# Performance work log

Measured on AMD Instinct MI355X. Metric: run time of the kernel, lower is better.

## Reference

```python
import jax, jax.numpy as jnp
import numpy as np

D_EMB = 1024
N_HEAD = 16
D_K = D_EMB // N_HEAD


def setup_inputs() -> dict:
    key = jax.random.key(0)
    ks = jax.random.split(key, 11)
    B, S = 2, 2048
    s = 1.0 / np.sqrt(D_EMB)
    inp = {
        'Q': jax.random.normal(ks[0], (B, S, D_EMB), jnp.float32),
        'K': jax.random.normal(ks[1], (B, S, D_EMB), jnp.float32),
        'V': jax.random.normal(ks[2], (B, S, D_EMB), jnp.float32),
        'W_Q': jax.random.normal(ks[3], (D_EMB, D_EMB), jnp.float32) * s,
        'b_Q': jax.random.normal(ks[4], (D_EMB,), jnp.float32) * s,
        'W_K': jax.random.normal(ks[5], (D_EMB, D_EMB), jnp.float32) * s,
        'b_K': jax.random.normal(ks[6], (D_EMB,), jnp.float32) * s,
        'W_V': jax.random.normal(ks[7], (D_EMB, D_EMB), jnp.float32) * s,
        'b_V': jax.random.normal(ks[8], (D_EMB,), jnp.float32) * s,
        'W_O': jax.random.normal(ks[9], (D_EMB, D_EMB), jnp.float32) * s,
        'b_O': jax.random.normal(ks[10], (D_EMB,), jnp.float32) * s,
    }
    return inp


def _heads(x):
    # [B, S, D] -> [B, H, S, d_k]
    B, S, _ = x.shape
    return x.reshape(B, S, N_HEAD, D_K).transpose(0, 2, 1, 3)


def reference(Q, K, V, W_Q, b_Q, W_K, b_K, W_V, b_V, W_O, b_O):
    q = _heads(Q @ W_Q.T + b_Q)
    k = _heads(K @ W_K.T + b_K)
    v = _heads(V @ W_V.T + b_V)
    scale = 1.0 / jnp.sqrt(jnp.asarray(D_K, q.dtype))
    scores = jnp.einsum('bhqd,bhkd->bhqk', q, k) * scale  # [B,H,S,S]
    probs = jax.nn.softmax(scores, axis=-1)
    attn = jnp.einsum('bhqk,bhkd->bhqd', probs, v)
    B, H, S, d = attn.shape
    attn = attn.transpose(0, 2, 1, 3).reshape(B, S, H * d)
    return attn @ W_O.T + b_O
```

## Files before the change

### kernel.cpp

```cpp
#include <hip/hip_runtime.h>
#include <cstdint>
#include <cstddef>

#define S_LEN 2048
#define NH    16
#define DKH   64
#define DEMB  1024
#define MTOT  4096
#define SLAB  (32 * S_LEN * DKH)

typedef float f32x4 __attribute__((ext_vector_type(4)));
typedef __bf16 bf16x8 __attribute__((ext_vector_type(8)));
typedef _Float16 f16;
typedef f16 f16x2 __attribute__((ext_vector_type(2)));
typedef f16 f16x4 __attribute__((ext_vector_type(4)));
typedef f16 f16x8 __attribute__((ext_vector_type(8)));
typedef unsigned short u16;
typedef unsigned int u32;
typedef u16 u16x8 __attribute__((ext_vector_type(8)));
typedef u16 u16x4 __attribute__((ext_vector_type(4)));
typedef u32 u32x4 __attribute__((ext_vector_type(4)));

static __device__ __forceinline__ u16 f2bf(float f) {
  u32 u = __builtin_bit_cast(u32, f);
  u += 0x7fffu + ((u >> 16) & 1u);
  return (u16)(u >> 16);
}
static __device__ __forceinline__ float bf2f(u16 b) {
  return __builtin_bit_cast(float, ((u32)b) << 16);
}
static __device__ __forceinline__ bf16x8 ldfrag(const u16* p) {
  return __builtin_bit_cast(bf16x8, *(const u16x8*)p);
}
static __device__ __forceinline__ f16x8 ldfragh8(const u16* p) {
  return __builtin_bit_cast(f16x8, *(const u16x8*)p);
}
static __device__ __forceinline__ f32x4 mfma16(bf16x8 a, bf16x8 b, f32x4 c) {
  return __builtin_amdgcn_mfma_f32_16x16x32_bf16(a, b, c, 0, 0, 0);
}
static __device__ __forceinline__ f32x4 mfmah32(f16x8 a, f16x8 b, f32x4 c) {
  return __builtin_amdgcn_mfma_f32_16x16x32_f16(a, b, c, 0, 0, 0);
}
static __device__ __forceinline__ void gl2lds16(const void* g, void* l) {
  __builtin_amdgcn_global_load_lds((__attribute__((address_space(1))) void*)g,
                                   (__attribute__((address_space(3))) void*)l,
                                   16, 0, 0);
}
static __device__ __forceinline__ u32 pkh2(float a, float b) {
  return __builtin_bit_cast(u32, __builtin_amdgcn_cvt_pkrtz(a, b));
}
static __device__ __forceinline__ f16x4 pkh4(float a, float b, float c, float d) {
  f16x2 lo = __builtin_bit_cast(f16x2, __builtin_amdgcn_cvt_pkrtz(a, b));
  f16x2 hi = __builtin_bit_cast(f16x2, __builtin_amdgcn_cvt_pkrtz(c, d));
  return __builtin_shufflevector(lo, hi, 0, 1, 2, 3);
}

#define SCL_Q (0.125f * 1.44269504088896340736f)

__global__ __launch_bounds__(256) void cvt_all(
    const float* __restrict__ wq, const float* __restrict__ wk,
    const float* __restrict__ wv, const float* __restrict__ wo,
    const float* __restrict__ q, const float* __restrict__ k,
    const float* __restrict__ v, u16* __restrict__ dW, u16* __restrict__ dA) {
  int b = blockIdx.x;
  const float* s; u16* d;
  if (b < 4096) {
    const int seg = b >> 10;
    s = (seg == 0) ? wq : (seg == 1) ? wk : (seg == 2) ? wv : wo;
    d = dW + (size_t)seg * (DEMB * DEMB);
    b &= 1023;
  } else {
    const int bb = b - 4096;
    const int seg = bb >> 12;
    s = (seg == 0) ? q : (seg == 1) ? k : v;
    d = dA + (size_t)seg * ((size_t)MTOT * DEMB);
    b = bb & 4095;
  }
  const int i = (b * 256 + threadIdx.x) * 4;
  f32x4 f = *(const f32x4*)(s + i);
  u16x4 o;
  o[0] = f2bf(f[0]); o[1] = f2bf(f[1]); o[2] = f2bf(f[2]); o[3] = f2bf(f[3]);
  *(u16x4*)(d + i) = o;
}

__global__ __launch_bounds__(256) void qkv_gemm(
    const u16* __restrict__ qin, const u16* __restrict__ kin,
    const u16* __restrict__ vin, const u16* __restrict__ W,
    const float* __restrict__ bq, const float* __restrict__ bk,
    const float* __restrict__ bv,
    u16* __restrict__ qh, u16* __restrict__ kh, u16* __restrict__ vt) {
  __shared__ __align__(16) u16 sA0[128 * 32], sA1[128 * 32];
  __shared__ __align__(16) u16 sB0[128 * 32], sB1[128 * 32];
  const int t = threadIdx.x;
  const int l = t & 63, w = t >> 6;
  const int ll = l & 15, lg = l >> 4;
  const int orig = blockIdx.x + 24 * blockIdx.y;
  const int xcd = orig & 7, q = orig >> 3;
  const int nb = q >> 2;
  const int mb = xcd * 4 + (q & 3);
  const int which = nb >> 3;
  const u16* A = (which == 0) ? qin : ((which == 1) ? kin : vin);
  const int wr = (w >> 1) * 64, wc = (w & 1) * 64;

  f32x4 acc[4][4] = {};

  auto stg = [&](int kt, u16* dA, u16* dB) {
    const int k0 = kt * 32;
#pragma unroll
    for (int i = 0; i < 2; ++i) {
      const int c = i * 256 + t;
      const int row = c >> 2;
      const int gc = (c & 3) ^ ((row >> 1) & 3);
      gl2lds16(A + (size_t)(mb * 128 + row) * DEMB + k0 + gc * 8, dA + c * 8);
      gl2lds16(W + (size_t)(nb * 128 + row) * DEMB + k0 + gc * 8, dB + c * 8);
    }
  };

  auto comp = [&](const u16* cA, const u16* cB) {
    bf16x8 af[4], bfr[4];
#pragma unroll
    for (int i2 = 0; i2 < 4; ++i2) {
      const int row = wr + i2 * 16 + ll;
      af[i2] = ldfrag(&cA[row * 32 + (lg ^ ((row >> 1) & 3)) * 8]);
    }
#pragma unroll
    for (int j2 = 0; j2 < 4; ++j2) {
      const int row = wc + j2 * 16 + ll;
      bfr[j2] = ldfrag(&cB[row * 32 + (lg ^ ((row >> 1) & 3)) * 8]);
    }
#pragma unroll
    for (int i2 = 0; i2 < 4; ++i2)
#pragma unroll
      for (int j2 = 0; j2 < 4; ++j2)
        acc[i2][j2] = mfma16(af[i2], bfr[j2], acc[i2][j2]);
  };

  stg(0, sA0, sB0);
  __syncthreads();
  for (int kt2 = 0; kt2 < 16; ++kt2) {
    stg(2 * kt2 + 1, sA1, sB1);
    comp(sA0, sB0);
    __syncthreads();
    if (kt2 < 15) stg(2 * kt2 + 2, sA0, sB0);
    comp(sA1, sB1);
    __syncthreads();
  }

  const float* bias = (which == 0) ? bq : ((which == 1) ? bk : bv);
  const int b = (mb * 128) >> 11;

  if (which == 2) {
#pragma unroll
    for (int j2 = 0; j2 < 4; ++j2) {
      const int nl = (nb * 128 + wc + j2 * 16 + ll) & 1023;
      const int h = nl >> 6, dk = nl & 63;
      const float bb = bias[nl];
      u16* base = vt + ((size_t)((b * NH + h) * DKH + dk)) * S_LEN;
#pragma unroll
      for (int i2 = 0; i2 < 4; ++i2) {
        const int s = (mb * 128 + wr + i2 * 16 + lg * 4) & 2047;
        const f16x4 pk = pkh4(acc[i2][j2][0] + bb, acc[i2][j2][1] + bb,
                              acc[i2][j2][2] + bb, acc[i2][j2][3] + bb);
        *(u16x4*)&base[s] = __builtin_bit_cast(u16x4, pk);
      }
    }
  } else {
    u16* outp = (which == 0) ? qh : kh;
    const float scl = (which == 0) ? SCL_Q : 1.0f;
#pragma unroll
    for (int j2 = 0; j2 < 4; ++j2) {
      const int nl = (nb * 128 + wc + j2 * 16 + ll) & 1023;
      const int h = nl >> 6, dk = nl & 63;
      const float bb = bias[nl];
#pragma unroll
      for (int i2 = 0; i2 < 4; ++i2) {
#pragma unroll
        for (int r = 0; r < 4; ++r) {
          const int s = (mb * 128 + wr + i2 * 16 + lg * 4 + r) & 2047;
          const float val = (acc[i2][j2][r] + bb) * scl;
          outp[((size_t)((b * NH + h) * S_LEN + s)) * DKH + dk] = f2bf(val);
        }
      }
    }
  }
}

__global__ __launch_bounds__(512, 4) void attn_kernel(
    const u16* __restrict__ qh, const u16* __restrict__ kh,
    const u16* __restrict__ vt, u16* __restrict__ opart,
    float* __restrict__ lpart) {
  __shared__ __align__(16) u16 sK0[64 * 64], sK1[64 * 64];
  __shared__ __align__(16) u16 sV0[64 * 64], sV1[64 * 64];
  const int t = threadIdx.x;
  const int l = t & 63, w = t >> 6;
  const int ll = l & 15, lg = l >> 4;
  const int qb = blockIdx.x >> 1;
  const int ks = blockIdx.x & 1;
  const int q_blk = qb * 256;
  const int bh = blockIdx.y;

  bf16x8 aq[2][2];
#pragma unroll
  for (int qt = 0; qt < 2; ++qt) {
    const u16* qbase =
        qh + ((size_t)bh * S_LEN + q_blk + w * 32 + qt * 16 + ll) * DKH;
    aq[qt][0] = ldfrag(qbase + lg * 8);
    aq[qt][1] = ldfrag(qbase + 32 + lg * 8);
  }

  f32x4 oT[2][4] = {};
  float l_part[2] = {0.f, 0.f};

  const int strow = t >> 3;
  const int sgc = (t & 7) ^ (strow & 7);
  const u16* kstg =
      kh + ((size_t)bh * S_LEN + ks * 1024 + strow) * DKH + sgc * 8;
  const u16* vstg =
      vt + ((size_t)bh * DKH + strow) * S_LEN + ks * 1024 + sgc * 8;

  auto stg = [&](int kt, u16* dK, u16* dV) {
    gl2lds16(kstg + (size_t)kt * 64 * DKH, dK + t * 8);
    gl2lds16(vstg + kt * 64, dV + t * 8);
  };

  auto compute = [&](const u16* cK, const u16* cV) {
#pragma unroll
    for (int pr = 0; pr < 2; ++pr) {
      u32 pw0[4], pw1[4];
#pragma unroll
      for (int h = 0; h < 2; ++h) {
        const int krow = (pr * 2 + h) * 16 + ll;
        const bf16x8 ak0 = ldfrag(&cK[krow * 64 + (lg ^ (ll & 7)) * 8]);
        const bf16x8 ak1 = ldfrag(&cK[krow * 64 + ((4 + lg) ^ (ll & 7)) * 8]);
        f32x4 s0 = {}, s1 = {};
        s0 = mfma16(ak0, aq[0][0], s0);
        s0 = mfma16(ak1, aq[0][1], s0);
        s1 = mfma16(ak0, aq[1][0], s1);
        s1 = mfma16(ak1, aq[1][1], s1);
        {
          const float p0 = __builtin_amdgcn_exp2f(s0[0]);
          const float p1 = __builtin_amdgcn_exp2f(s0[1]);
          const float p2 = __builtin_amdgcn_exp2f(s0[2]);
          const float p3 = __builtin_amdgcn_exp2f(s0[3]);
          l_part[0] += (p0 + p1) + (p2 + p3);
          if (h == 0) { pw0[0] = pkh2(p0, p1); pw0[1] = pkh2(p2, p3); }
          else        { pw0[2] = pkh2(p0, p1); pw0[3] = pkh2(p2, p3); }
        }
        {
          const float p0 = __builtin_amdgcn_exp2f(s1[0]);
          const float p1 = __builtin_amdgcn_exp2f(s1[1]);
          const float p2 = __builtin_amdgcn_exp2f(s1[2]);
          const float p3 = __builtin_amdgcn_exp2f(s1[3]);
          l_part[1] += (p0 + p1) + (p2 + p3);
          if (h == 0) { pw1[0] = pkh2(p0, p1); pw1[1] = pkh2(p2, p3); }
          else        { pw1[2] = pkh2(p0, p1); pw1[3] = pkh2(p2, p3); }
        }
      }
      asm volatile("v_permlane32_swap_b32 %0, %1" : "+v"(pw0[0]), "+v"(pw0[2]));
      asm volatile("v_permlane16_swap_b32 %0, %1" : "+v"(pw0[0]), "+v"(pw0[2]));
      asm volatile("v_permlane32_swap_b32 %0, %1" : "+v"(pw0[1]), "+v"(pw0[3]));
      asm volatile("v_permlane16_swap_b32 %0, %1" : "+v"(pw0[1]), "+v"(pw0[3]));
      asm volatile("v_permlane32_swap_b32 %0, %1" : "+v"(pw1[0]), "+v"(pw1[2]));
      asm volatile("v_permlane16_swap_b32 %0, %1" : "+v"(pw1[0]), "+v"(pw1[2]));
      asm volatile("v_permlane32_swap_b32 %0, %1" : "+v"(pw1[1]), "+v"(pw1[3]));
      asm volatile("v_permlane16_swap_b32 %0, %1" : "+v"(pw1[1]), "+v"(pw1[3]));
      const f16x8 bp0 =
          __builtin_bit_cast(f16x8, (u32x4){pw0[0], pw0[1], pw0[2], pw0[3]});
      const f16x8 bp1 =
          __builtin_bit_cast(f16x8, (u32x4){pw1[0], pw1[1], pw1[2], pw1[3]});

#pragma unroll
      for (int nt = 0; nt < 4; ++nt) {
        const int row = nt * 16 + ll;
        const f16x8 av =
            ldfragh8(&cV[row * 64 + ((pr * 4 + lg) ^ (ll & 7)) * 8]);
        oT[0][nt] = mfmah32(av, bp0, oT[0][nt]);
        oT[1][nt] = mfmah32(av, bp1, oT[1][nt]);
      }
    }
  };

  stg(0, sK0, sV0);
  __syncthreads();
  for (int kt2 = 0; kt2 < 8; ++kt2) {
    stg(2 * kt2 + 1, sK1, sV1);
    compute(sK0, sV0);
    __syncthreads();
    if (kt2 < 7) stg(2 * kt2 + 2, sK0, sV0);
    compute(sK1, sV1);
    __syncthreads();
  }

#pragma unroll
  for (int qt = 0; qt < 2; ++qt) {
    float lv = l_part[qt];
    lv += __shfl_xor(lv, 16, 64);
    lv += __shfl_xor(lv, 32, 64);
    const int orow = q_blk + w * 32 + qt * 16 + ll;
    u16* obase = opart + (((size_t)(ks * 32 + bh)) * S_LEN + orow) * DKH;
#pragma unroll
    for (int nt = 0; nt < 4; ++nt) {
      u16x4 o;
#pragma unroll
      for (int r = 0; r < 4; ++r) o[r] = f2bf(oT[qt][nt][r]);
      *(u16x4*)&obase[nt * 16 + lg * 4] = o;
    }
    if (lg == 0) lpart[(ks * 32 + bh) * S_LEN + orow] = lv;
  }
}

__global__ __launch_bounds__(256) void merge_ctx(
    const u16* __restrict__ op, const float* __restrict__ lp,
    u16* __restrict__ ctx) {
  const int idx = blockIdx.x * 256 + threadIdx.x;
  const int dk8 = idx & 7;
  const int q = (idx >> 3) & 2047;
  const int bh = idx >> 14;
  const float inv = 1.0f / (lp[bh * S_LEN + q] + lp[(32 + bh) * S_LEN + q]);
  const u16x8 a = *(const u16x8*)&op[((size_t)bh * S_LEN + q) * DKH + dk8 * 8];
  const u16x8 c = *(const u16x8*)&op[((size_t)(32 + bh) * S_LEN + q) * DKH + dk8 * 8];
  u16x8 o;
#pragma unroll
  for (int r = 0; r < 8; ++r) o[r] = f2bf((bf2f(a[r]) + bf2f(c[r])) * inv);
  const int b = bh >> 4, h = bh & 15;
  *(u16x8*)&ctx[((size_t)((b * S_LEN + q) * NH + h)) * DKH + dk8 * 8] = o;
}

__global__ __launch_bounds__(256) void out_gemm(
    const u16* __restrict__ Am, const u16* __restrict__ W,
    const float* __restrict__ bo, float* __restrict__ out) {
  __shared__ __align__(16) u16 sA0[128 * 64], sA1[128 * 64];
  __shared__ __align__(16) u16 sB0[64 * 64], sB1[64 * 64];
  const int t = threadIdx.x;
  const int l = t & 63, w = t >> 6;
  const int ll = l & 15, lg = l >> 4;
  const int nb = blockIdx.x;
  const int mb = blockIdx.y;
  const int wr = (w >> 1) * 64, wc = (w & 1) * 32;

  f32x4 acc[4][2] = {};

  auto stg = [&](int kt, u16* dA, u16* dB) {
    const int k0 = kt * 64;
#pragma unroll
    for (int i = 0; i < 4; ++i) {
      const int c = i * 256 + t;
      const int row = c >> 3;
      const int gc = (c & 7) ^ (row & 7);
      gl2lds16(Am + (size_t)(mb * 128 + row) * DEMB + k0 + gc * 8, dA + c * 8);
      if (i < 2)
        gl2lds16(W + (size_t)(nb * 64 + row) * DEMB + k0 + gc * 8, dB + c * 8);
    }
  };

  auto comp = [&](const u16* cA, const u16* cB) {
#pragma unroll
    for (int kk = 0; kk < 2; ++kk) {
      bf16x8 af[4], bfr[2];
#pragma unroll
      for (int i2 = 0; i2 < 4; ++i2) {
        const int row = wr + i2 * 16 + ll;
        af[i2] = ldfrag(&cA[row * 64 + ((kk * 4 + lg) ^ (row & 7)) * 8]);
      }
#pragma unroll
      for (int j2 = 0; j2 < 2; ++j2) {
        const int row = wc + j2 * 16 + ll;
        bfr[j2] = ldfrag(&cB[row * 64 + ((kk * 4 + lg) ^ (row & 7)) * 8]);
      }
#pragma unroll
      for (int i2 = 0; i2 < 4; ++i2)
#pragma unroll
        for (int j2 = 0; j2 < 2; ++j2)
          acc[i2][j2] = mfma16(af[i2], bfr[j2], acc[i2][j2]);
    }
  };

  stg(0, sA0, sB0);
  __syncthreads();
  for (int kt2 = 0; kt2 < 8; ++kt2) {
    stg(2 * kt2 + 1, sA1, sB1);
    comp(sA0, sB0);
    __syncthreads();
    if (kt2 < 7) stg(2 * kt2 + 2, sA0, sB0);
    comp(sA1, sB1);
    __syncthreads();
  }

#pragma unroll
  for (int j2 = 0; j2 < 2; ++j2) {
    const int ncol = nb * 64 + wc + j2 * 16 + ll;
    const float bb = bo[ncol];
#pragma unroll
    for (int i2 = 0; i2 < 4; ++i2) {
#pragma unroll
      for (int r = 0; r < 4; ++r) {
        const int mrow = mb * 128 + wr + i2 * 16 + lg * 4 + r;
        out[(size_t)mrow * DEMB + ncol] = acc[i2][j2][r] + bb;
      }
    }
  }
}

extern "C" void kernel_launch(void* const* d_in, const int* in_sizes, int n_in,
                              void* d_out, int out_size, void* d_ws,
                              size_t ws_size, hipStream_t stream) {
  (void)in_sizes; (void)n_in; (void)out_size; (void)ws_size;
  const float* Q  = (const float*)d_in[0];
  const float* K  = (const float*)d_in[1];
  const float* V  = (const float*)d_in[2];
  const float* WQ = (const float*)d_in[3];
  const float* bQ = (const float*)d_in[4];
  const float* WK = (const float*)d_in[5];
  const float* bK = (const float*)d_in[6];
  const float* WV = (const float*)d_in[7];
  const float* bV = (const float*)d_in[8];
  const float* WO = (const float*)d_in[9];
  const float* bO = (const float*)d_in[10];
  float* out = (float*)d_out;

  u16* ws   = (u16*)d_ws;
  u16* Wqkv = ws;
  u16* Wo   = Wqkv + 3072 * 1024;
  u16* qin  = Wo + 1024 * 1024;
  u16* kin  = qin + (size_t)MTOT * DEMB;
  u16* vin  = kin + (size_t)MTOT * DEMB;
  u16* qh   = vin + (size_t)MTOT * DEMB;
  u16* kh   = qh + 32 * 2048 * 64;
  u16* vt   = kh + 32 * 2048 * 64;
  u16* ctx  = vt + 32 * 2048 * 64;
  u16* opart   = qin;
  float* lpart = (float*)Wqkv;

  cvt_all<<<16384, 256, 0, stream>>>(WQ, WK, WV, WO, Q, K, V, Wqkv, qin);

  qkv_gemm<<<dim3(24, 32), 256, 0, stream>>>(qin, kin, vin, Wqkv, bQ, bK, bV,
                                             qh, kh, vt);
  attn_kernel<<<dim3(16, 32), 512, 0, stream>>>(qh, kh, vt, opart, lpart);
  merge_ctx<<<2048, 256, 0, stream>>>(opart, lpart, ctx);
  out_gemm<<<dim3(16, 32), 256, 0, stream>>>(ctx, Wo, bO, out);
}
```

Measured before the change: 222.6 us.

## Split attention keys four ways and halve QKV GEMM N-tile for more blocks

The QKV projection GEMM now uses 128x64 tiles instead of 128x128, doubling the grid to 1536 blocks. The attention kernel splits the key range into four 512-key chunks instead of two, launching 1024 blocks, and merge_ctx sums four partial outputs and four partial row sums. The fourth partial slab is stored in the output buffer's scratch space because the workspace is full. The goal is better CU occupancy and load balance on the many-CU device, at the cost of extra partial-output traffic in the merge and less operand reuse per GEMM tile.

New measurement: 234.6 us. 1.05x slower.

```diff
diff --git a/kernel.cpp b/kernel.cpp
--- a/kernel.cpp
+++ b/kernel.cpp
@@ -90,19 +90,19 @@
     const float* __restrict__ bv,
     u16* __restrict__ qh, u16* __restrict__ kh, u16* __restrict__ vt) {
   __shared__ __align__(16) u16 sA0[128 * 32], sA1[128 * 32];
-  __shared__ __align__(16) u16 sB0[128 * 32], sB1[128 * 32];
+  __shared__ __align__(16) u16 sB0[64 * 32],  sB1[64 * 32];
   const int t = threadIdx.x;
   const int l = t & 63, w = t >> 6;
   const int ll = l & 15, lg = l >> 4;
-  const int orig = blockIdx.x + 24 * blockIdx.y;
+  const int orig = blockIdx.x + 48 * blockIdx.y;
   const int xcd = orig & 7, q = orig >> 3;
-  const int nb = q >> 2;
-  const int mb = xcd * 4 + (q & 3);
-  const int which = nb >> 3;
+  const int nb = q % 48;
+  const int mb = xcd * 4 + (q / 48);
+  const int which = nb >> 4;
   const u16* A = (which == 0) ? qin : ((which == 1) ? kin : vin);
-  const int wr = (w >> 1) * 64, wc = (w & 1) * 64;
-
-  f32x4 acc[4][4] = {};
+  const int wr = (w >> 1) * 64, wc = (w & 1) * 32;
+
+  f32x4 acc[4][2] = {};
 
   auto stg = [&](int kt, u16* dA, u16* dB) {
     const int k0 = kt * 32;
@@ -112,26 +112,31 @@
       const int row = c >> 2;
       const int gc = (c & 3) ^ ((row >> 1) & 3);
       gl2lds16(A + (size_t)(mb * 128 + row) * DEMB + k0 + gc * 8, dA + c * 8);
-      gl2lds16(W + (size_t)(nb * 128 + row) * DEMB + k0 + gc * 8, dB + c * 8);
+    }
+    {
+      const int c = t;
+      const int row = c >> 2;
+      const int gc = (c & 3) ^ ((row >> 1) & 3);
+      gl2lds16(W + (size_t)(nb * 64 + row) * DEMB + k0 + gc * 8, dB + c * 8);
     }
   };
 
   auto comp = [&](const u16* cA, const u16* cB) {
-    bf16x8 af[4], bfr[4];
+    bf16x8 af[4], bfr[2];
 #pragma unroll
     for (int i2 = 0; i2 < 4; ++i2) {
       const int row = wr + i2 * 16 + ll;
       af[i2] = ldfrag(&cA[row * 32 + (lg ^ ((row >> 1) & 3)) * 8]);
     }
 #pragma unroll
-    for (int j2 = 0; j2 < 4; ++j2) {
+    for (int j2 = 0; j2 < 2; ++j2) {
       const int row = wc + j2 * 16 + ll;
       bfr[j2] = ldfrag(&cB[row * 32 + (lg ^ ((row >> 1) & 3)) * 8]);
     }
 #pragma unroll
     for (int i2 = 0; i2 < 4; ++i2)
 #pragma unroll
-      for (int j2 = 0; j2 < 4; ++j2)
+      for (int j2 = 0; j2 < 2; ++j2)
         acc[i2][j2] = mfma16(af[i2], bfr[j2], acc[i2][j2]);
   };
 
@@ -151,8 +156,8 @@
 
   if (which == 2) {
 #pragma unroll
-    for (int j2 = 0; j2 < 4; ++j2) {
-      const int nl = (nb * 128 + wc + j2 * 16 + ll) & 1023;
+    for (int j2 = 0; j2 < 2; ++j2) {
+      const int nl = (nb * 64 + wc + j2 * 16 + ll) & 1023;
       const int h = nl >> 6, dk = nl & 63;
       const float bb = bias[nl];
       u16* base = vt + ((size_t)((b * NH + h) * DKH + dk)) * S_LEN;
@@ -168,8 +173,8 @@
     u16* outp = (which == 0) ? qh : kh;
     const float scl = (which == 0) ? SCL_Q : 1.0f;
 #pragma unroll
-    for (int j2 = 0; j2 < 4; ++j2) {
-      const int nl = (nb * 128 + wc + j2 * 16 + ll) & 1023;
+    for (int j2 = 0; j2 < 2; ++j2) {
+      const int nl = (nb * 64 + wc + j2 * 16 + ll) & 1023;
       const int h = nl >> 6, dk = nl & 63;
       const float bb = bias[nl];
 #pragma unroll
@@ -187,15 +192,15 @@
 
 __global__ __launch_bounds__(512, 4) void attn_kernel(
     const u16* __restrict__ qh, const u16* __restrict__ kh,
-    const u16* __restrict__ vt, u16* __restrict__ opart,
+    const u16* __restrict__ vt, u16* __restrict__ opA, u16* __restrict__ opB,
     float* __restrict__ lpart) {
   __shared__ __align__(16) u16 sK0[64 * 64], sK1[64 * 64];
   __shared__ __align__(16) u16 sV0[64 * 64], sV1[64 * 64];
   const int t = threadIdx.x;
   const int l = t & 63, w = t >> 6;
   const int ll = l & 15, lg = l >> 4;
-  const int qb = blockIdx.x >> 1;
-  const int ks = blockIdx.x & 1;
+  const int qb = blockIdx.x >> 2;
+  const int ks = blockIdx.x & 3;
   const int q_blk = qb * 256;
   const int bh = blockIdx.y;
 
@@ -214,9 +219,9 @@
   const int strow = t >> 3;
   const int sgc = (t & 7) ^ (strow & 7);
   const u16* kstg =
-      kh + ((size_t)bh * S_LEN + ks * 1024 + strow) * DKH + sgc * 8;
+      kh + ((size_t)bh * S_LEN + ks * 512 + strow) * DKH + sgc * 8;
   const u16* vstg =
-      vt + ((size_t)bh * DKH + strow) * S_LEN + ks * 1024 + sgc * 8;
+      vt + ((size_t)bh * DKH + strow) * S_LEN + ks * 512 + sgc * 8;
 
   auto stg = [&](int kt, u16* dK, u16* dV) {
     gl2lds16(kstg + (size_t)kt * 64 * DKH, dK + t * 8);
@@ -282,22 +287,23 @@
 
   stg(0, sK0, sV0);
   __syncthreads();
-  for (int kt2 = 0; kt2 < 8; ++kt2) {
+  for (int kt2 = 0; kt2 < 4; ++kt2) {
     stg(2 * kt2 + 1, sK1, sV1);
     compute(sK0, sV0);
     __syncthreads();
-    if (kt2 < 7) stg(2 * kt2 + 2, sK0, sV0);
+    if (kt2 < 3) stg(2 * kt2 + 2, sK0, sV0);
     compute(sK1, sV1);
     __syncthreads();
   }
 
+  u16* oslab = (ks < 3) ? (opA + (size_t)ks * SLAB) : opB;
 #pragma unroll
   for (int qt = 0; qt < 2; ++qt) {
     float lv = l_part[qt];
     lv += __shfl_xor(lv, 16, 64);
     lv += __shfl_xor(lv, 32, 64);
     const int orow = q_blk + w * 32 + qt * 16 + ll;
-    u16* obase = opart + (((size_t)(ks * 32 + bh)) * S_LEN + orow) * DKH;
+    u16* obase = oslab + ((size_t)bh * S_LEN + orow) * DKH;
 #pragma unroll
     for (int nt = 0; nt < 4; ++nt) {
       u16x4 o;
@@ -310,18 +316,23 @@
 }
 
 __global__ __launch_bounds__(256) void merge_ctx(
-    const u16* __restrict__ op, const float* __restrict__ lp,
-    u16* __restrict__ ctx) {
+    const u16* __restrict__ opA, const u16* __restrict__ opB,
+    const float* __restrict__ lp, u16* __restrict__ ctx) {
   const int idx = blockIdx.x * 256 + threadIdx.x;
   const int dk8 = idx & 7;
   const int q = (idx >> 3) & 2047;
   const int bh = idx >> 14;
-  const float inv = 1.0f / (lp[bh * S_LEN + q] + lp[(32 + bh) * S_LEN + q]);
-  const u16x8 a = *(const u16x8*)&op[((size_t)bh * S_LEN + q) * DKH + dk8 * 8];
-  const u16x8 c = *(const u16x8*)&op[((size_t)(32 + bh) * S_LEN + q) * DKH + dk8 * 8];
+  const float inv = 1.0f / (lp[bh * S_LEN + q] + lp[(32 + bh) * S_LEN + q] +
+                            lp[(64 + bh) * S_LEN + q] + lp[(96 + bh) * S_LEN + q]);
+  const size_t base = ((size_t)bh * S_LEN + q) * DKH + dk8 * 8;
+  const u16x8 a  = *(const u16x8*)&opA[base];
+  const u16x8 b2 = *(const u16x8*)&opA[base + SLAB];
+  const u16x8 c  = *(const u16x8*)&opA[base + 2 * (size_t)SLAB];
+  const u16x8 d  = *(const u16x8*)&opB[base];
   u16x8 o;
 #pragma unroll
-  for (int r = 0; r < 8; ++r) o[r] = f2bf((bf2f(a[r]) + bf2f(c[r])) * inv);
+  for (int r = 0; r < 8; ++r)
+    o[r] = f2bf(((bf2f(a[r]) + bf2f(b2[r])) + (bf2f(c[r]) + bf2f(d[r]))) * inv);
   const int b = bh >> 4, h = bh & 15;
   *(u16x8*)&ctx[((size_t)((b * S_LEN + q) * NH + h)) * DKH + dk8 * 8] = o;
 }
@@ -428,14 +439,15 @@
   u16* kh   = qh + 32 * 2048 * 64;
   u16* vt   = kh + 32 * 2048 * 64;
   u16* ctx  = vt + 32 * 2048 * 64;
-  u16* opart   = qin;
+  u16* opA  = qin;
+  u16* opB  = (u16*)out + (size_t)SLAB;
   float* lpart = (float*)Wqkv;
 
   cvt_all<<<16384, 256, 0, stream>>>(WQ, WK, WV, WO, Q, K, V, Wqkv, qin);
 
-  qkv_gemm<<<dim3(24, 32), 256, 0, stream>>>(qin, kin, vin, Wqkv, bQ, bK, bV,
+  qkv_gemm<<<dim3(48, 32), 256, 0, stream>>>(qin, kin, vin, Wqkv, bQ, bK, bV,
                                              qh, kh, vt);
-  attn_kernel<<<dim3(16, 32), 512, 0, stream>>>(qh, kh, vt, opart, lpart);
-  merge_ctx<<<2048, 256, 0, stream>>>(opart, lpart, ctx);
+  attn_kernel<<<dim3(32, 32), 512, 0, stream>>>(qh, kh, vt, opA, opB, lpart);
+  merge_ctx<<<2048, 256, 0, stream>>>(opA, opB, lpart, ctx);
   out_gemm<<<dim3(16, 32), 256, 0, stream>>>(ctx, Wo, bO, out);
 }
```

## Fuse fp32-to-bf16 activation conversion into QKV GEMM and move Wo conversion into merge

Applied to the files above, without the earlier changes.

The QKV GEMM now reads the fp32 Q/K/V activations directly, converting them to bf16 in registers and storing them into swizzled LDS. This drops the separate conversion pass that wrote 3x4096x1024 bf16 copies and read them back. Converting W_O moves into extra blocks of merge_ctx, so the standalone conversion kernel only handles the three QKV weights. In exchange, the GEMM's A loads are twice as wide and go through registers instead of direct global-to-LDS loads, which may expose load latency in the K loop. The workspace layout is also reorganised so the partial outputs no longer alias the input buffers.

Result: slower. 247.6 us (+11.2%).

```diff
diff --git a/kernel.cpp b/kernel.cpp
--- a/kernel.cpp
+++ b/kernel.cpp
@@ -7,7 +7,6 @@
 #define DKH   64
 #define DEMB  1024
 #define MTOT  4096
-#define SLAB  (32 * S_LEN * DKH)
 
 typedef float f32x4 __attribute__((ext_vector_type(4)));
 typedef __bf16 bf16x8 __attribute__((ext_vector_type(8)));
@@ -57,26 +56,14 @@
 
 #define SCL_Q (0.125f * 1.44269504088896340736f)
 
-__global__ __launch_bounds__(256) void cvt_all(
+__global__ __launch_bounds__(256) void cvt_w(
     const float* __restrict__ wq, const float* __restrict__ wk,
-    const float* __restrict__ wv, const float* __restrict__ wo,
-    const float* __restrict__ q, const float* __restrict__ k,
-    const float* __restrict__ v, u16* __restrict__ dW, u16* __restrict__ dA) {
-  int b = blockIdx.x;
-  const float* s; u16* d;
-  if (b < 4096) {
-    const int seg = b >> 10;
-    s = (seg == 0) ? wq : (seg == 1) ? wk : (seg == 2) ? wv : wo;
-    d = dW + (size_t)seg * (DEMB * DEMB);
-    b &= 1023;
-  } else {
-    const int bb = b - 4096;
-    const int seg = bb >> 12;
-    s = (seg == 0) ? q : (seg == 1) ? k : v;
-    d = dA + (size_t)seg * ((size_t)MTOT * DEMB);
-    b = bb & 4095;
-  }
-  const int i = (b * 256 + threadIdx.x) * 4;
+    const float* __restrict__ wv, u16* __restrict__ dW) {
+  const int b = blockIdx.x;
+  const int seg = b >> 10;
+  const float* s = (seg == 0) ? wq : (seg == 1) ? wk : wv;
+  u16* d = dW + (size_t)seg * (DEMB * DEMB);
+  const int i = ((b & 1023) * 256 + threadIdx.x) * 4;
   f32x4 f = *(const f32x4*)(s + i);
   u16x4 o;
   o[0] = f2bf(f[0]); o[1] = f2bf(f[1]); o[2] = f2bf(f[2]); o[3] = f2bf(f[3]);
@@ -84,8 +71,8 @@
 }
 
 __global__ __launch_bounds__(256) void qkv_gemm(
-    const u16* __restrict__ qin, const u16* __restrict__ kin,
-    const u16* __restrict__ vin, const u16* __restrict__ W,
+    const float* __restrict__ qf, const float* __restrict__ kf,
+    const float* __restrict__ vf, const u16* __restrict__ W,
     const float* __restrict__ bq, const float* __restrict__ bk,
     const float* __restrict__ bv,
     u16* __restrict__ qh, u16* __restrict__ kh, u16* __restrict__ vt) {
@@ -99,21 +86,43 @@
   const int nb = q >> 2;
   const int mb = xcd * 4 + (q & 3);
   const int which = nb >> 3;
-  const u16* A = (which == 0) ? qin : ((which == 1) ? kin : vin);
+  const float* A = (which == 0) ? qf : ((which == 1) ? kf : vf);
   const int wr = (w >> 1) * 64, wc = (w & 1) * 64;
 
   f32x4 acc[4][4] = {};
 
-  auto stg = [&](int kt, u16* dA, u16* dB) {
+  const int c0 = t, c1 = 256 + t;
+  const int row0 = c0 >> 2, row1 = c1 >> 2;
+  const int gc0 = (c0 & 3) ^ ((row0 >> 1) & 3);
+  const int gc1 = (c1 & 3) ^ ((row1 >> 1) & 3);
+  const float* asrc0 = A + (size_t)(mb * 128 + row0) * DEMB + gc0 * 8;
+  const float* asrc1 = A + (size_t)(mb * 128 + row1) * DEMB + gc1 * 8;
+  const u16* bsrc0 = W + (size_t)(nb * 128 + row0) * DEMB + gc0 * 8;
+  const u16* bsrc1 = W + (size_t)(nb * 128 + row1) * DEMB + gc1 * 8;
+
+  f32x4 va[4];
+  auto LOADA = [&](int kt) {
     const int k0 = kt * 32;
+    va[0] = *(const f32x4*)(asrc0 + k0);
+    va[1] = *(const f32x4*)(asrc0 + k0 + 4);
+    va[2] = *(const f32x4*)(asrc1 + k0);
+    va[3] = *(const f32x4*)(asrc1 + k0 + 4);
+  };
+  auto STOREA = [&](u16* dA) {
 #pragma unroll
     for (int i = 0; i < 2; ++i) {
-      const int c = i * 256 + t;
-      const int row = c >> 2;
-      const int gc = (c & 3) ^ ((row >> 1) & 3);
-      gl2lds16(A + (size_t)(mb * 128 + row) * DEMB + k0 + gc * 8, dA + c * 8);
-      gl2lds16(W + (size_t)(nb * 128 + row) * DEMB + k0 + gc * 8, dB + c * 8);
-    }
+      u16x8 o;
+#pragma unroll
+      for (int r = 0; r < 4; ++r) o[r] = f2bf(va[2 * i][r]);
+#pragma unroll
+      for (int r = 0; r < 4; ++r) o[4 + r] = f2bf(va[2 * i + 1][r]);
+      *(u16x8*)&dA[(i * 256 + t) * 8] = o;
+    }
+  };
+  auto STGB = [&](int kt, u16* dB) {
+    const int k0 = kt * 32;
+    gl2lds16(bsrc0 + k0, dB + c0 * 8);
+    gl2lds16(bsrc1 + k0, dB + c1 * 8);
   };
 
   auto comp = [&](const u16* cA, const u16* cB) {
@@ -135,14 +144,17 @@
         acc[i2][j2] = mfma16(af[i2], bfr[j2], acc[i2][j2]);
   };
 
-  stg(0, sA0, sB0);
+  LOADA(0); STGB(0, sB0); STOREA(sA0);
   __syncthreads();
   for (int kt2 = 0; kt2 < 16; ++kt2) {
-    stg(2 * kt2 + 1, sA1, sB1);
+    LOADA(2 * kt2 + 1);
+    STGB(2 * kt2 + 1, sB1);
     comp(sA0, sB0);
-    __syncthreads();
-    if (kt2 < 15) stg(2 * kt2 + 2, sA0, sB0);
+    STOREA(sA1);
+    __syncthreads();
+    if (kt2 < 15) { LOADA(2 * kt2 + 2); STGB(2 * kt2 + 2, sB0); }
     comp(sA1, sB1);
+    if (kt2 < 15) STOREA(sA0);
     __syncthreads();
   }
 
@@ -311,7 +323,16 @@
 
 __global__ __launch_bounds__(256) void merge_ctx(
     const u16* __restrict__ op, const float* __restrict__ lp,
-    u16* __restrict__ ctx) {
+    u16* __restrict__ ctx, const float* __restrict__ wo,
+    u16* __restrict__ woBf) {
+  if (blockIdx.x >= 2048) {
+    const int i = ((blockIdx.x - 2048) * 256 + threadIdx.x) * 4;
+    f32x4 f = *(const f32x4*)(wo + i);
+    u16x4 o;
+    o[0] = f2bf(f[0]); o[1] = f2bf(f[1]); o[2] = f2bf(f[2]); o[3] = f2bf(f[3]);
+    *(u16x4*)(woBf + i) = o;
+    return;
+  }
   const int idx = blockIdx.x * 256 + threadIdx.x;
   const int dk8 = idx & 7;
   const int q = (idx >> 3) & 2047;
@@ -420,22 +441,18 @@
 
   u16* ws   = (u16*)d_ws;
   u16* Wqkv = ws;
-  u16* Wo   = Wqkv + 3072 * 1024;
-  u16* qin  = Wo + 1024 * 1024;
-  u16* kin  = qin + (size_t)MTOT * DEMB;
-  u16* vin  = kin + (size_t)MTOT * DEMB;
-  u16* qh   = vin + (size_t)MTOT * DEMB;
-  u16* kh   = qh + 32 * 2048 * 64;
-  u16* vt   = kh + 32 * 2048 * 64;
-  u16* ctx  = vt + 32 * 2048 * 64;
-  u16* opart   = qin;
-  float* lpart = (float*)Wqkv;
-
-  cvt_all<<<16384, 256, 0, stream>>>(WQ, WK, WV, WO, Q, K, V, Wqkv, qin);
-
-  qkv_gemm<<<dim3(24, 32), 256, 0, stream>>>(qin, kin, vin, Wqkv, bQ, bK, bV,
+  u16* WoBf = Wqkv + (size_t)3072 * 1024;
+  u16* qh   = WoBf + (size_t)1024 * 1024;
+  u16* kh   = qh + (size_t)32 * 2048 * 64;
+  u16* vt   = kh + (size_t)32 * 2048 * 64;
+  u16* ctx  = vt + (size_t)32 * 2048 * 64;
+  u16* opart   = ctx + (size_t)MTOT * DEMB;
+  float* lpart = (float*)(opart + (size_t)2 * 32 * 2048 * 64);
+
+  cvt_w<<<3072, 256, 0, stream>>>(WQ, WK, WV, Wqkv);
+  qkv_gemm<<<dim3(24, 32), 256, 0, stream>>>(Q, K, V, Wqkv, bQ, bK, bV,
                                              qh, kh, vt);
   attn_kernel<<<dim3(16, 32), 512, 0, stream>>>(qh, kh, vt, opart, lpart);
-  merge_ctx<<<2048, 256, 0, stream>>>(opart, lpart, ctx);
-  out_gemm<<<dim3(16, 32), 256, 0, stream>>>(ctx, Wo, bO, out);
-}
+  merge_ctx<<<3072, 256, 0, stream>>>(opart, lpart, ctx, WO, WoBf);
+  out_gemm<<<dim3(16, 32), 256, 0, stream>>>(ctx, WoBf, bO, out);
+}
```
